# Optimization experiments

Measured on AMD Instinct MI355X. Metric: run time of the kernel, lower is better.

## Reference

```python
import jax, jax.numpy as jnp
import numpy as np

EPS = 1e-6


def setup_inputs() -> dict:
    key = jax.random.key(0)
    k1, k2 = jax.random.split(key)
    S, B, H, F = 4096, 8, 1024, 1024
    x = jax.random.normal(k1, (S, B, H), dtype=jnp.float32)
    scale = jnp.ones((H,), dtype=jnp.float32)
    ln_bias = jnp.zeros((H,), dtype=jnp.float32)
    # variance_scaling(1.0, 'fan_in', 'truncated_normal') ~ normal with std 1/sqrt(fan_in)
    kernel = jax.random.normal(k2, (H, F), dtype=jnp.float32) * (1.0 / np.sqrt(H))
    return {"x": x, "scale": scale, "ln_bias": ln_bias, "kernel": kernel}


def reference(x, scale, ln_bias, kernel):
    # LayerNorm over last (hidden) axis; zero_centered_gamma=False:
    #   y = (x - mean) / sqrt(var + eps) * gamma + beta
    mu = jnp.mean(x, axis=-1, keepdims=True)
    var = jnp.mean(jnp.square(x - mu), axis=-1, keepdims=True)
    ln_out = (x - mu) * jax.lax.rsqrt(var + EPS) * scale + ln_bias
    # DenseGeneral: contract hidden axis with kernel (H, F); use_bias=False, no depth scaling
    out = jnp.einsum("sbh,hf->sbf", ln_out, kernel)
    # return_layernorm_output=True -> (out, ln_out)
    return (out, ln_out)
```

## Files before the change

### kernel.cpp

```cpp
#include <hip/hip_runtime.h>
#include <stdint.h>

typedef unsigned short u16;

#define S_ 4096
#define B_ 8
#define H_ 1024
#define F_ 1024
#define M_ (S_ * B_)
#define N_ F_
#define K_ H_

#define BM 128
#define BN 128
#define BK 64

typedef short short8 __attribute__((ext_vector_type(8)));
typedef float floatx4 __attribute__((ext_vector_type(4)));

__device__ __forceinline__ u16 f2bf(float f) {
    union { float f; uint32_t u; } c;
    c.f = f;
    uint32_t u = c.u;
    uint32_t r = (u + 0x7fffu + ((u >> 16) & 1u)) >> 16;
    return (u16)r;
}

__device__ __forceinline__ void async_load16(const void* gptr, void* lptr) {
    __builtin_amdgcn_global_load_lds(
        (const __attribute__((address_space(1))) uint32_t*)gptr,
        (__attribute__((address_space(3))) uint32_t*)lptr,
        16 , 0 , 0 );
}

__global__ __launch_bounds__(256) void transpose_cast_kernel(
    const float* __restrict__ w, u16* __restrict__ bt)
{
    __shared__ float tile[32][33];
    const int tx = threadIdx.x;
    const int ty = threadIdx.y;
    const int n0 = blockIdx.x * 32;
    const int k0 = blockIdx.y * 32;
#pragma unroll
    for (int j = 0; j < 4; ++j)
        tile[ty + j * 8][tx] = w[(size_t)(k0 + ty + j * 8) * N_ + n0 + tx];
    __syncthreads();
#pragma unroll
    for (int j = 0; j < 4; ++j)
        bt[(size_t)(n0 + ty + j * 8) * K_ + k0 + tx] =
            f2bf(tile[tx][ty + j * 8]);
}

__global__ __launch_bounds__(256) void ln_kernel(
    const float* __restrict__ x, const float* __restrict__ scale,
    const float* __restrict__ bias, float* __restrict__ ln_out,
    u16* __restrict__ ln_bf16)
{
    const int row = blockIdx.x;
    const int tid = threadIdx.x;
    const float4 v = reinterpret_cast<const float4*>(x + (size_t)row * H_)[tid];

    float s  = v.x + v.y + v.z + v.w;
    float sq = v.x * v.x + v.y * v.y + v.z * v.z + v.w * v.w;
#pragma unroll
    for (int off = 32; off >= 1; off >>= 1) {
        s  += __shfl_down(s, off, 64);
        sq += __shfl_down(sq, off, 64);
    }
    __shared__ float red[8];
    const int wave = tid >> 6, lane = tid & 63;
    if (lane == 0) { red[wave] = s; red[4 + wave] = sq; }
    __syncthreads();
    const float Ssum = red[0] + red[1] + red[2] + red[3];
    const float Qsum = red[4] + red[5] + red[6] + red[7];
    const float mu   = Ssum * (1.0f / H_);
    const float var  = Qsum * (1.0f / H_) - mu * mu;
    const float rstd = rsqrtf(var + 1e-6f);

    const float4 sc = reinterpret_cast<const float4*>(scale)[tid];
    const float4 bi = reinterpret_cast<const float4*>(bias)[tid];
    float4 y;
    y.x = (v.x - mu) * rstd * sc.x + bi.x;
    y.y = (v.y - mu) * rstd * sc.y + bi.y;
    y.z = (v.z - mu) * rstd * sc.z + bi.z;
    y.w = (v.w - mu) * rstd * sc.w + bi.w;

    reinterpret_cast<float4*>(ln_out + (size_t)row * H_)[tid] = y;

    ushort4 h;
    h.x = f2bf(y.x); h.y = f2bf(y.y); h.z = f2bf(y.z); h.w = f2bf(y.w);
    reinterpret_cast<ushort4*>(ln_bf16 + (size_t)row * H_)[tid] = h;
}

__global__ __launch_bounds__(256, 2) void gemm_bt_kernel(
    const u16* __restrict__ A, const u16* __restrict__ Bt,
    float* __restrict__ C)
{
    __shared__ __align__(16) u16 As[BM * BK];
    __shared__ __align__(16) u16 Bs[BN * BK];

    const int tid  = threadIdx.x;
    const int wave = tid >> 6;
    const int lane = tid & 63;
    const int wm   = wave >> 1;
    const int wn   = wave & 1;
    const int row0 = blockIdx.y * BM;
    const int col0 = blockIdx.x * BN;

    floatx4 acc[4][4];
#pragma unroll
    for (int i = 0; i < 4; ++i)
#pragma unroll
        for (int j = 0; j < 4; ++j) acc[i][j] = (floatx4)0.0f;

    const int srow = wave * 8 + (lane >> 3);
    const int scol = (lane & 7) * 8;
    const u16* Ag = A + (size_t)(row0 + srow) * K_ + scol;
    const u16* Bg = Bt + (size_t)(col0 + srow) * K_ + scol;
    char* AsBase = (char*)As + (size_t)(wave * 8) * (BK * 2);
    char* BsBase = (char*)Bs + (size_t)(wave * 8) * (BK * 2);

    for (int kt = 0; kt < K_ / BK; ++kt) {
        const int k0 = kt * BK;
#pragma unroll
        for (int i = 0; i < 4; ++i) {
            async_load16(Ag + (size_t)(i * 32) * K_ + k0,
                         AsBase + (size_t)(i * 32) * (BK * 2));
            async_load16(Bg + (size_t)(i * 32) * K_ + k0,
                         BsBase + (size_t)(i * 32) * (BK * 2));
        }
        __syncthreads();

#pragma unroll
        for (int ks = 0; ks < 2; ++ks) {
            const int kb = ks * 32 + (lane >> 4) * 8;
            short8 af[4], bf[4];
#pragma unroll
            for (int mt = 0; mt < 4; ++mt)
                af[mt] = *reinterpret_cast<const short8*>(
                    &As[(wm * 64 + mt * 16 + (lane & 15)) * BK + kb]);
#pragma unroll
            for (int nt = 0; nt < 4; ++nt)
                bf[nt] = *reinterpret_cast<const short8*>(
                    &Bs[(wn * 64 + nt * 16 + (lane & 15)) * BK + kb]);
#pragma unroll
            for (int mt = 0; mt < 4; ++mt)
#pragma unroll
                for (int nt = 0; nt < 4; ++nt)
                    acc[mt][nt] = __builtin_amdgcn_mfma_f32_16x16x32_bf16(
                        af[mt], bf[nt], acc[mt][nt], 0, 0, 0);
        }
        __syncthreads();
    }

#pragma unroll
    for (int mt = 0; mt < 4; ++mt) {
#pragma unroll
        for (int nt = 0; nt < 4; ++nt) {
            const int r0 = row0 + wm * 64 + mt * 16 + (lane >> 4) * 4;
            const int c  = col0 + wn * 64 + nt * 16 + (lane & 15);
#pragma unroll
            for (int r = 0; r < 4; ++r)
                C[(size_t)(r0 + r) * N_ + c] = acc[mt][nt][r];
        }
    }
}

extern "C" void kernel_launch(void* const* d_in, const int* in_sizes, int n_in,
                              void* d_out, int out_size, void* d_ws, size_t ws_size,
                              hipStream_t stream) {
    const float* x      = (const float*)d_in[0];
    const float* scale  = (const float*)d_in[1];
    const float* lnbias = (const float*)d_in[2];
    const float* weight = (const float*)d_in[3];

    float* out    = (float*)d_out;
    float* ln_out = (float*)d_out + (size_t)M_ * N_;

    u16* ln_bf16 = (u16*)d_ws;
    u16* bt      = (u16*)d_ws + (size_t)M_ * K_;

    transpose_cast_kernel<<<dim3(N_ / 32, K_ / 32), dim3(32, 8), 0, stream>>>(
        weight, bt);
    ln_kernel<<<M_, 256, 0, stream>>>(x, scale, lnbias, ln_out, ln_bf16);
    gemm_bt_kernel<<<dim3(N_ / BN, M_ / BM), 256, 0, stream>>>(ln_bf16, bt, out);
}
```

Measured before the change: 444.0 us.

## Swizzle GEMM LDS layout, remap block order for L2 reuse, relax launch bounds

The GEMM's shared-memory tiles now use an XOR swizzle. Each thread's global source column is permuted by row so the async global-to-LDS loads place 16-byte chunks at swizzled positions, and the MFMA fragment reads apply the matching XOR to avoid LDS bank conflicts. The launch becomes a 1D grid remapped so groups of 8 row-tiles sweep all 8 column-tiles together, which is meant to improve L2 reuse of A and B. The min-blocks-per-CU hint of 2 is dropped, giving the compiler more register freedom at possible cost to occupancy.

```diff
diff --git a/kernel.cpp b/kernel.cpp
--- a/kernel.cpp
+++ b/kernel.cpp
@@ -92,7 +92,7 @@
     reinterpret_cast<ushort4*>(ln_bf16 + (size_t)row * H_)[tid] = h;
 }
 
-__global__ __launch_bounds__(256, 2) void gemm_bt_kernel(
+__global__ __launch_bounds__(256) void gemm_bt_kernel(
     const u16* __restrict__ A, const u16* __restrict__ Bt,
     float* __restrict__ C)
 {
@@ -104,8 +104,12 @@
     const int lane = tid & 63;
     const int wm   = wave >> 1;
     const int wn   = wave & 1;
-    const int row0 = blockIdx.y * BM;
-    const int col0 = blockIdx.x * BN;
+
+    const int bid  = blockIdx.x;
+    const int bx   = (bid >> 3) & 7;
+    const int by   = ((bid >> 6) << 3) | (bid & 7);
+    const int row0 = by * BM;
+    const int col0 = bx * BN;
 
     floatx4 acc[4][4];
 #pragma unroll
@@ -114,7 +118,7 @@
         for (int j = 0; j < 4; ++j) acc[i][j] = (floatx4)0.0f;
 
     const int srow = wave * 8 + (lane >> 3);
-    const int scol = (lane & 7) * 8;
+    const int scol = (((lane & 7) ^ (lane >> 3)) * 8);
     const u16* Ag = A + (size_t)(row0 + srow) * K_ + scol;
     const u16* Bg = Bt + (size_t)(col0 + srow) * K_ + scol;
     char* AsBase = (char*)As + (size_t)(wave * 8) * (BK * 2);
@@ -133,16 +137,23 @@
 
 #pragma unroll
         for (int ks = 0; ks < 2; ++ks) {
-            const int kb = ks * 32 + (lane >> 4) * 8;
             short8 af[4], bf[4];
 #pragma unroll
-            for (int mt = 0; mt < 4; ++mt)
+            for (int mt = 0; mt < 4; ++mt) {
+                const int r = wm * 64 + mt * 16 + (lane & 15);
+                const int q = ks * 4 + (lane >> 4);
+                const int c = q ^ (r & 7);
                 af[mt] = *reinterpret_cast<const short8*>(
-                    &As[(wm * 64 + mt * 16 + (lane & 15)) * BK + kb]);
+                    (const char*)As + (size_t)r * (BK * 2) + c * 16);
+            }
 #pragma unroll
-            for (int nt = 0; nt < 4; ++nt)
+            for (int nt = 0; nt < 4; ++nt) {
+                const int r = wn * 64 + nt * 16 + (lane & 15);
+                const int q = ks * 4 + (lane >> 4);
+                const int c = q ^ (r & 7);
                 bf[nt] = *reinterpret_cast<const short8*>(
-                    &Bs[(wn * 64 + nt * 16 + (lane & 15)) * BK + kb]);
+                    (const char*)Bs + (size_t)r * (BK * 2) + c * 16);
+            }
 #pragma unroll
             for (int mt = 0; mt < 4; ++mt)
 #pragma unroll
@@ -183,5 +194,5 @@
     transpose_cast_kernel<<<dim3(N_ / 32, K_ / 32), dim3(32, 8), 0, stream>>>(
         weight, bt);
     ln_kernel<<<M_, 256, 0, stream>>>(x, scale, lnbias, ln_out, ln_bf16);
-    gemm_bt_kernel<<<dim3(N_ / BN, M_ / BM), 256, 0, stream>>>(ln_bf16, bt, out);
+    gemm_bt_kernel<<<(M_ / BM) * (N_ / BN), 256, 0, stream>>>(ln_bf16, bt, out);
 }
```

Result: faster. 430.5 us (-3.0%).
